# Kernel optimization log

Measured on AMD Instinct MI355X. Metric: run time of the kernel, lower is better.

## Reference

```python
import jax, jax.numpy as jnp
import numpy as np

B, T, HID = 2, 2048, 2048
NH, NKV, D = 16, 4, 128
WIN = 512
ROPE_BASE = 10000.0
SCALE = D ** -0.5
EPS = 1e-12


def setup_inputs() -> dict:
    key = jax.random.key(0)
    ks = jax.random.split(key, 5)
    x = jax.random.normal(ks[0], (B, T, HID), dtype=jnp.float32)
    wq = jax.random.normal(ks[1], (HID, NH * D), dtype=jnp.float32) * 0.02
    wk = jax.random.normal(ks[2], (HID, NKV * D), dtype=jnp.float32) * 0.02
    wv = jax.random.normal(ks[3], (HID, NKV * D), dtype=jnp.float32) * 0.02
    wo = jax.random.normal(ks[4], (NH * D, HID), dtype=jnp.float32) * 0.02
    return {"x": x, "wq": wq, "wk": wk, "wv": wv, "wo": wo}


def _rope_tables(t, offset=0):
    inv_freq = 1.0 / (ROPE_BASE ** (jnp.arange(0, D, 2, dtype=jnp.float32) / D))
    pos = jnp.arange(offset, offset + t, dtype=jnp.float32)
    freqs = pos[:, None] * inv_freq[None, :]              # [t, D/2]
    cos = jnp.concatenate([jnp.cos(freqs), jnp.cos(freqs)], axis=-1)  # [t, D]
    sin = jnp.concatenate([jnp.sin(freqs), jnp.sin(freqs)], axis=-1)
    return cos, sin


def _apply_rope(x, cos, sin):
    # x: [B, H, T, D]; rotate-half formulation
    x1, x2 = jnp.split(x, 2, axis=-1)
    rot = jnp.concatenate([-x2, x1], axis=-1)
    return x * cos[None, None] + rot * sin[None, None]


def _l2norm(x):
    n = jnp.sqrt(jnp.sum(x * x, axis=-1, keepdims=True))
    return x / jnp.maximum(n, EPS)


def _forward(x, wq, wk, wv, wo):
    b, t, _ = x.shape
    q = (x @ wq).reshape(b, t, NH, D).transpose(0, 2, 1, 3)    # [B,H,T,D]
    k = (x @ wk).reshape(b, t, NKV, D).transpose(0, 2, 1, 3)   # [B,Hk,T,D]
    v = (x @ wv).reshape(b, t, NKV, D).transpose(0, 2, 1, 3)
    q = _l2norm(q)
    k = _l2norm(k)
    cos, sin = _rope_tables(t, offset=0)
    q = _apply_rope(q, cos, sin)
    k = _apply_rope(k, cos, sin)
    rep = NH // NKV
    k = jnp.repeat(k, rep, axis=1)                             # GQA repeat_interleave
    v = jnp.repeat(v, rep, axis=1)
    i = jnp.arange(t)
    allowed = (i[None, :] <= i[:, None]) & (i[None, :] > i[:, None] - WIN)  # [T,T]
    logits = jnp.einsum("bhid,bhjd->bhij", q, k) * SCALE
    logits = jnp.where(allowed[None, None], logits, -jnp.inf)
    attn = jax.nn.softmax(logits, axis=-1)
    out = jnp.einsum("bhij,bhjd->bhid", attn, v)
    out = out.transpose(0, 2, 1, 3).reshape(b, t, NH * D)
    return out @ wo


def reference(x, wq, wk, wv, wo):
    return _forward(x, wq, wk, wv, wo)
```

## Files before the change

### kernel.cpp

```cpp
#include <hip/hip_runtime.h>
#include <hip/hip_bf16.h>
#include <cstdint>

#define NHQ 16
#define NKVH 4
#define HDIM 128
#define WINSZ 512
#define TSEQ 2048
#define ATTN_SCALE 0.08838834764831845f

typedef __attribute__((ext_vector_type(8))) short s16x8;
typedef __attribute__((ext_vector_type(4))) float f32x4;

__device__ __forceinline__ void gload16(const void* g, void* lds) {
  __builtin_amdgcn_global_load_lds(
      (const __attribute__((address_space(1))) unsigned int*)g,
      (__attribute__((address_space(3))) unsigned int*)(uintptr_t)lds,
      16, 0, 0);
}

__device__ __forceinline__ f32x4 mfma16(s16x8 a, s16x8 b, f32x4 c) {
  return __builtin_amdgcn_mfma_f32_16x16x32_bf16(a, b, c, 0, 0, 0);
}

#define SBAR() asm volatile("s_barrier" ::: "memory")
#define VMCNT(n) asm volatile("s_waitcnt vmcnt(" #n ")" ::: "memory")

__global__ __launch_bounds__(256) void rope_tables_kernel(float* __restrict__ cosT,
                                                          float* __restrict__ sinT) {
  int idx = blockIdx.x * 256 + threadIdx.x;
  int t = idx >> 6, d2 = idx & 63;
  float inv = powf(10000.0f, -(float)d2 / 64.0f);
  float a = (float)t * inv;
  cosT[idx] = cosf(a);
  sinT[idx] = sinf(a);
}

__global__ __launch_bounds__(256) void cast_kernel(const float* __restrict__ in,
                                                   __bf16* __restrict__ out, int n4) {
  int i = blockIdx.x * 256 + threadIdx.x;
  if (i >= n4) return;
  float4 v = ((const float4*)in)[i];
  union { __bf16 h[4]; uint2 u; } pk;
  pk.h[0] = (__bf16)v.x; pk.h[1] = (__bf16)v.y; pk.h[2] = (__bf16)v.z; pk.h[3] = (__bf16)v.w;
  ((uint2*)out)[i] = pk.u;
}

__global__ __launch_bounds__(256) void transpose_cast(const float* __restrict__ in,
                                                      __bf16* __restrict__ out, int R, int C) {
  __shared__ float tile[32][33];
  int c0 = blockIdx.x * 32, r0 = blockIdx.y * 32;
  int tx = threadIdx.x, ty = threadIdx.y;
#pragma unroll
  for (int i = 0; i < 4; i++)
    tile[ty + i * 8][tx] = in[(size_t)(r0 + ty + i * 8) * C + c0 + tx];
  __syncthreads();
#pragma unroll
  for (int i = 0; i < 4; i++)
    out[(size_t)(c0 + ty + i * 8) * R + r0 + tx] = (__bf16)tile[tx][ty + i * 8];
}

template <int MODE>
__global__ __launch_bounds__(512, 2) void gemm256(const __bf16* __restrict__ A,
                                                  const __bf16* __restrict__ Bt,
                                                  float* __restrict__ Cf,
                                                  __bf16* __restrict__ Qo, __bf16* __restrict__ Ko,
                                                  __bf16* __restrict__ Vo, int M, int N, int K) {
  __shared__ __attribute__((aligned(16))) char Lds[3][2][16384];

  const int tid = threadIdx.x;
  const int w = tid >> 6, lane = tid & 63;
  const int wm = w >> 2, wn = w & 3;

  const int nbx = gridDim.x;
  const int nwg = nbx * gridDim.y;
  const int bid = blockIdx.y * nbx + blockIdx.x;
  const int q8 = nwg >> 3, r8 = nwg & 7;
  const int xcd = bid & 7, idx = bid >> 3;
  const int swz = (xcd < r8 ? xcd * (q8 + 1) : r8 * (q8 + 1) + (xcd - r8) * q8) + idx;
  const int bx = swz % nbx, by = swz / nbx;
  const int m0 = by * 256, n0 = bx * 256;

  const int r_st = tid >> 2;
  const int c_src = (tid & 3) ^ ((tid >> 3) & 3);
  const __bf16* gA = A + (size_t)(m0 + r_st) * K + c_src * 8;
  const __bf16* gB = Bt + (size_t)(n0 + r_st) * K + c_src * 8;
  const size_t hOF = (size_t)128 * K;

  auto stA = [&](int t, int h, int b) {
    gload16(gA + h * hOF + t * 32, Lds[b][0] + h * 8192 + w * 1024);
  };
  auto stB = [&](int t, int h, int b) {
    gload16(gB + h * hOF + t * 32, Lds[b][1] + h * 8192 + w * 1024);
  };

  const int swzr = (((lane >> 4) ^ (((lane & 15) >> 1) & 3)) << 4);
  const int aoff = wm * 8192 + (lane & 15) * 64 + swzr;
  const int boff = (wn >> 1) * 8192 + (wn & 1) * 4096 + (lane & 15) * 64 + swzr;

  f32x4 acc[8][4];
  f32x4 zero = {0.f, 0.f, 0.f, 0.f};
#pragma unroll
  for (int i = 0; i < 8; i++)
#pragma unroll
    for (int j = 0; j < 4; j++) acc[i][j] = zero;

  const int NT = K >> 5;

  stA(0, 0, 0); stA(0, 1, 0); stB(0, 0, 0); stB(0, 1, 0);
  stA(1, 0, 1); stA(1, 1, 1); stB(1, 0, 1);
  VMCNT(3);
  SBAR();

  int cur = 0;
  for (int t = 0; t < NT; ++t) {
    int nb1 = cur + 1; if (nb1 == 3) nb1 = 0;
    int nb2 = nb1 + 1; if (nb2 == 3) nb2 = 0;
    const char* bA = Lds[cur][0];
    const char* bB = Lds[cur][1];

    s16x8 fb[4], fa[4];
#pragma unroll
    for (int nf = 0; nf < 4; nf++) fb[nf] = *(const s16x8*)(bB + boff + nf * 1024);
#pragma unroll
    for (int mf = 0; mf < 4; mf++) fa[mf] = *(const s16x8*)(bA + aoff + mf * 1024);
    if (t + 1 < NT) stB(t + 1, 1, nb1);
    if (t + 2 < NT) stA(t + 2, 0, nb2);
    SBAR();
    __builtin_amdgcn_s_setprio(1);
#pragma unroll
    for (int mf = 0; mf < 4; mf++)
#pragma unroll
      for (int nf = 0; nf < 4; nf++) acc[mf][nf] = mfma16(fa[mf], fb[nf], acc[mf][nf]);
    __builtin_amdgcn_s_setprio(0);
    SBAR();

#pragma unroll
    for (int mf = 0; mf < 4; mf++) fa[mf] = *(const s16x8*)(bA + aoff + 4096 + mf * 1024);
    if (t + 2 < NT) { stA(t + 2, 1, nb2); stB(t + 2, 0, nb2); }
    SBAR();
    __builtin_amdgcn_s_setprio(1);
#pragma unroll
    for (int mf = 0; mf < 4; mf++)
#pragma unroll
      for (int nf = 0; nf < 4; nf++) acc[4 + mf][nf] = mfma16(fa[mf], fb[nf], acc[4 + mf][nf]);
    __builtin_amdgcn_s_setprio(0);

    if (t < NT - 2) {
      VMCNT(3);
      SBAR();
    } else if (t == NT - 2) {
      VMCNT(0);
      SBAR();
    }
    cur = nb1;
  }

#pragma unroll
  for (int mf = 0; mf < 8; mf++)
#pragma unroll
    for (int nf = 0; nf < 4; nf++) {
      int rbase = m0 + wm * 128 + mf * 16 + (lane >> 4) * 4;
      int col = n0 + wn * 64 + nf * 16 + (lane & 15);
#pragma unroll
      for (int r = 0; r < 4; r++) {
        int m = rbase + r;
        float v = acc[mf][nf][r];
        if constexpr (MODE == 0) {
          Cf[(size_t)m * N + col] = v;
        } else {
          int b = m >> 11, t = m & 2047;
          __bf16 bv = (__bf16)v;
          if (col < 2048) {
            Qo[(((size_t)(b * NHQ + (col >> 7))) * TSEQ + t) * HDIM + (col & 127)] = bv;
          } else if (col < 2560) {
            int c2 = col - 2048;
            Ko[(((size_t)(b * NKVH + (c2 >> 7))) * TSEQ + t) * HDIM + (c2 & 127)] = bv;
          } else {
            int c2 = col - 2560;
            Vo[(((size_t)(b * NKVH + (c2 >> 7))) * TSEQ + t) * HDIM + (c2 & 127)] = bv;
          }
        }
      }
    }
}

__global__ __launch_bounds__(256) void normrope(__bf16* __restrict__ Q, __bf16* __restrict__ Kk,
                                                const float* __restrict__ cosT,
                                                const float* __restrict__ sinT) {
  int w = threadIdx.x >> 6, lane = threadIdx.x & 63;
  int row = blockIdx.x / 5;
  int slot = (blockIdx.x % 5) * 4 + w;
  int b = row >> 11, t = row & 2047;
  __bf16* p;
  if (slot < 16)
    p = Q + (((size_t)(b * NHQ + slot)) * TSEQ + t) * HDIM;
  else
    p = Kk + (((size_t)(b * NKVH + (slot - 16))) * TSEQ + t) * HDIM;
  float x1 = (float)p[lane], x2 = (float)p[lane + 64];
  float ss = x1 * x1 + x2 * x2;
#pragma unroll
  for (int off = 32; off; off >>= 1) ss += __shfl_xor(ss, off);
  float inv = 1.0f / fmaxf(sqrtf(ss), 1e-12f);
  x1 *= inv;
  x2 *= inv;
  float c = cosT[t * 64 + lane], s = sinT[t * 64 + lane];
  p[lane] = (__bf16)(x1 * c - x2 * s);
  p[lane + 64] = (__bf16)(x2 * c + x1 * s);
}

__global__ __launch_bounds__(256) void attn_kernel(const __bf16* __restrict__ Qf,
                                                   const __bf16* __restrict__ Kf,
                                                   const __bf16* __restrict__ Vf,
                                                   __bf16* __restrict__ Ab) {
  __shared__ __align__(16) __bf16 Kl[32 * 136];
  __shared__ __align__(16) __bf16 Vt[128 * 40];
  __shared__ __align__(16) __bf16 Pl[4][16 * 40];
  int tid = threadIdx.x, w = tid >> 6, lane = tid & 63;
  int bid = blockIdx.x;
  int qt = bid & 31, h = (bid >> 5) & 15, b = bid >> 9;
  int qs = qt * 64;
  int kvh = h >> 2;
  const __bf16* Qb = Qf + ((size_t)(b * NHQ + h) * TSEQ) * HDIM;
  const __bf16* Kb = Kf + ((size_t)(b * NKVH + kvh) * TSEQ) * HDIM;
  const __bf16* Vb = Vf + ((size_t)(b * NKVH + kvh) * TSEQ) * HDIM;

  s16x8 aq[4];
  int qrow_f = qs + w * 16 + (lane & 15);
#pragma unroll
  for (int kb = 0; kb < 4; kb++)
    aq[kb] = *(const s16x8*)(Qb + (size_t)qrow_f * HDIM + kb * 32 + (lane >> 4) * 8);

  f32x4 acc[8];
  f32x4 zero = {0.f, 0.f, 0.f, 0.f};
#pragma unroll
  for (int db = 0; db < 8; db++) acc[db] = zero;
  float mrow[4], lrow[4];
#pragma unroll
  for (int r = 0; r < 4; r++) { mrow[r] = -1e30f; lrow[r] = 0.f; }

  int lo = qs - (WINSZ - 1);
  if (lo < 0) lo = 0;
  lo &= ~31;

  for (int ks = lo; ks <= qs + 63; ks += 32) {
    __syncthreads();
#pragma unroll
    for (int i = 0; i < 2; i++) {
      int c = tid + 256 * i;
      int j = c >> 4, dk = (c & 15) * 8;
      int4 kv = *(const int4*)(Kb + (size_t)(ks + j) * HDIM + dk);
      *(int4*)&Kl[j * 136 + dk] = kv;
      int jv = c & 31, d0 = (c >> 5) * 8;
      int4 vv = *(const int4*)(Vb + (size_t)(ks + jv) * HDIM + d0);
      const __bf16* pv = (const __bf16*)&vv;
#pragma unroll
      for (int e = 0; e < 8; e++) Vt[(d0 + e) * 40 + jv] = pv[e];
    }
    __syncthreads();

    f32x4 sacc[2];
    sacc[0] = zero; sacc[1] = zero;
#pragma unroll
    for (int jb = 0; jb < 2; jb++)
#pragma unroll
      for (int kb = 0; kb < 4; kb++) {
        s16x8 bk = *(const s16x8*)&Kl[(jb * 16 + (lane & 15)) * 136 + kb * 32 + (lane >> 4) * 8];
        sacc[jb] = mfma16(aq[kb], bk, sacc[jb]);
      }

    int colbase = ks + (lane & 15);
    float p0v[4], p1v[4], scf[4];
#pragma unroll
    for (int r = 0; r < 4; r++) {
      int qrow = qs + w * 16 + (lane >> 4) * 4 + r;
      float s0 = sacc[0][r] * ATTN_SCALE, s1 = sacc[1][r] * ATTN_SCALE;
      int j0 = colbase, j1 = colbase + 16;
      bool a0 = (j0 <= qrow) && (j0 > qrow - WINSZ);
      bool a1 = (j1 <= qrow) && (j1 > qrow - WINSZ);
      float mt = fmaxf(a0 ? s0 : -1e30f, a1 ? s1 : -1e30f);
#pragma unroll
      for (int off = 1; off < 16; off <<= 1) mt = fmaxf(mt, __shfl_xor(mt, off));
      float mn = fmaxf(mrow[r], mt);
      float p0 = a0 ? __expf(s0 - mn) : 0.f;
      float p1 = a1 ? __expf(s1 - mn) : 0.f;
      float sf = __expf(mrow[r] - mn);
      float ts = p0 + p1;
#pragma unroll
      for (int off = 1; off < 16; off <<= 1) ts += __shfl_xor(ts, off);
      lrow[r] = lrow[r] * sf + ts;
      mrow[r] = mn;
      p0v[r] = p0; p1v[r] = p1; scf[r] = sf;
    }

#pragma unroll
    for (int r = 0; r < 4; r++) {
      Pl[w][((lane >> 4) * 4 + r) * 40 + 0 * 16 + (lane & 15)] = (__bf16)p0v[r];
      Pl[w][((lane >> 4) * 4 + r) * 40 + 1 * 16 + (lane & 15)] = (__bf16)p1v[r];
    }
#pragma unroll
    for (int db = 0; db < 8; db++) {
      f32x4 t = acc[db];
#pragma unroll
      for (int r = 0; r < 4; r++) t[r] *= scf[r];
      acc[db] = t;
    }

    s16x8 pa = *(const s16x8*)&Pl[w][(lane & 15) * 40 + (lane >> 4) * 8];
#pragma unroll
    for (int db = 0; db < 8; db++) {
      s16x8 bv = *(const s16x8*)&Vt[(db * 16 + (lane & 15)) * 40 + (lane >> 4) * 8];
      acc[db] = mfma16(pa, bv, acc[db]);
    }
  }

#pragma unroll
  for (int db = 0; db < 8; db++)
#pragma unroll
    for (int r = 0; r < 4; r++) {
      int qrow = qs + w * 16 + (lane >> 4) * 4 + r;
      float v = acc[db][r] / lrow[r];
      Ab[((size_t)(b * TSEQ + qrow)) * 2048 + h * HDIM + db * 16 + (lane & 15)] = (__bf16)v;
    }
}

extern "C" void kernel_launch(void* const* d_in, const int* in_sizes, int n_in,
                              void* d_out, int out_size, void* d_ws, size_t ws_size,
                              hipStream_t stream) {
  const float* x = (const float*)d_in[0];
  const float* wq = (const float*)d_in[1];
  const float* wk = (const float*)d_in[2];
  const float* wv = (const float*)d_in[3];
  const float* wo = (const float*)d_in[4];
  float* out = (float*)d_out;

  char* ws = (char*)d_ws;
  size_t off = 0;
  auto alloc = [&](size_t bytes) -> void* {
    void* p = ws + off;
    off += (bytes + 255) & ~(size_t)255;
    return p;
  };
  __bf16* Xb = (__bf16*)alloc((size_t)4096 * 2048 * 2);
  __bf16* Wqkvt = (__bf16*)alloc((size_t)3072 * 2048 * 2);
  __bf16* Wot = (__bf16*)alloc((size_t)2048 * 2048 * 2);
  __bf16* Q = (__bf16*)alloc((size_t)2 * NHQ * TSEQ * HDIM * 2);
  __bf16* Kb = (__bf16*)alloc((size_t)2 * NKVH * TSEQ * HDIM * 2);
  __bf16* Vb = (__bf16*)alloc((size_t)2 * NKVH * TSEQ * HDIM * 2);
  float* cosT = (float*)alloc((size_t)TSEQ * 64 * 4);
  float* sinT = (float*)alloc((size_t)TSEQ * 64 * 4);
  __bf16* Ab = Xb;

  rope_tables_kernel<<<TSEQ * 64 / 256, 256, 0, stream>>>(cosT, sinT);
  cast_kernel<<<8192, 256, 0, stream>>>(x, Xb, 2097152);
  dim3 tb(32, 8);
  transpose_cast<<<dim3(64, 64), tb, 0, stream>>>(wq, Wqkvt, 2048, 2048);
  transpose_cast<<<dim3(16, 64), tb, 0, stream>>>(wk, Wqkvt + (size_t)2048 * 2048, 2048, 512);
  transpose_cast<<<dim3(16, 64), tb, 0, stream>>>(wv, Wqkvt + (size_t)2560 * 2048, 2048, 512);
  transpose_cast<<<dim3(64, 64), tb, 0, stream>>>(wo, Wot, 2048, 2048);

  gemm256<1><<<dim3(12, 16), 512, 0, stream>>>(Xb, Wqkvt, nullptr, Q, Kb, Vb, 4096, 3072, 2048);
  normrope<<<4096 * 5, 256, 0, stream>>>(Q, Kb, cosT, sinT);
  attn_kernel<<<2 * NHQ * (TSEQ / 64), 256, 0, stream>>>(Q, Kb, Vb, Ab);
  gemm256<0><<<dim3(8, 16), 512, 0, stream>>>(Ab, Wot, out, nullptr, nullptr, nullptr, 4096, 2048,
                                              2048);
}
```

Measured before the change: 240.4 us.

## Deepen GEMM pipeline to four LDS stages and narrow output-projection tiles

The GEMM kernel now uses four LDS buffers with a prefetch distance of three K-steps instead of three buffers and distance two, and waits on vmcnt values derived from the per-step load count. It is also templated on the N-fragment count, so the output projection runs with 256x128 tiles and a 256-workgroup grid in place of 128 workgroups. This targets memory latency and poor CU occupancy on the smaller GEMM. In exchange it uses more LDS per workgroup, which may limit residency of two blocks per CU, and the narrower tiles reuse A less.

```diff
diff --git a/kernel.cpp b/kernel.cpp
--- a/kernel.cpp
+++ b/kernel.cpp
@@ -25,6 +25,15 @@
 
 #define SBAR() asm volatile("s_barrier" ::: "memory")
 #define VMCNT(n) asm volatile("s_waitcnt vmcnt(" #n ")" ::: "memory")
+
+template <int N>
+__device__ __forceinline__ void vmwait() {
+  if constexpr (N == 8) VMCNT(8);
+  else if constexpr (N == 6) VMCNT(6);
+  else if constexpr (N == 4) VMCNT(4);
+  else if constexpr (N == 3) VMCNT(3);
+  else VMCNT(0);
+}
 
 __global__ __launch_bounds__(256) void rope_tables_kernel(float* __restrict__ cosT,
                                                           float* __restrict__ sinT) {
@@ -60,13 +69,16 @@
     out[(size_t)(c0 + ty + i * 8) * R + r0 + tx] = (__bf16)tile[tx][ty + i * 8];
 }
 
-template <int MODE>
+template <int MODE, int NF>
 __global__ __launch_bounds__(512, 2) void gemm256(const __bf16* __restrict__ A,
                                                   const __bf16* __restrict__ Bt,
                                                   float* __restrict__ Cf,
                                                   __bf16* __restrict__ Qo, __bf16* __restrict__ Ko,
                                                   __bf16* __restrict__ Vo, int M, int N, int K) {
-  __shared__ __attribute__((aligned(16))) char Lds[3][2][16384];
+  constexpr int BUNITS = NF / 2;
+  constexpr int LPT = 2 + BUNITS;
+  constexpr int STEADY = 2 * LPT;
+  __shared__ __attribute__((aligned(16))) char Lds[4][(2 + BUNITS) * 8192];
 
   const int tid = threadIdx.x;
   const int w = tid >> 6, lane = tid & 63;
@@ -79,7 +91,7 @@
   const int xcd = bid & 7, idx = bid >> 3;
   const int swz = (xcd < r8 ? xcd * (q8 + 1) : r8 * (q8 + 1) + (xcd - r8) * q8) + idx;
   const int bx = swz % nbx, by = swz / nbx;
-  const int m0 = by * 256, n0 = bx * 256;
+  const int m0 = by * 256, n0 = bx * (NF * 64);
 
   const int r_st = tid >> 2;
   const int c_src = (tid & 3) ^ ((tid >> 3) & 3);
@@ -88,80 +100,88 @@
   const size_t hOF = (size_t)128 * K;
 
   auto stA = [&](int t, int h, int b) {
-    gload16(gA + h * hOF + t * 32, Lds[b][0] + h * 8192 + w * 1024);
+    gload16(gA + h * hOF + t * 32, Lds[b] + h * 8192 + w * 1024);
   };
-  auto stB = [&](int t, int h, int b) {
-    gload16(gB + h * hOF + t * 32, Lds[b][1] + h * 8192 + w * 1024);
+  auto stB = [&](int t, int u, int b) {
+    gload16(gB + u * hOF + t * 32, Lds[b] + 16384 + u * 8192 + w * 1024);
   };
 
   const int swzr = (((lane >> 4) ^ (((lane & 15) >> 1) & 3)) << 4);
   const int aoff = wm * 8192 + (lane & 15) * 64 + swzr;
-  const int boff = (wn >> 1) * 8192 + (wn & 1) * 4096 + (lane & 15) * 64 + swzr;
-
-  f32x4 acc[8][4];
+  const int boff = (NF == 4 ? ((wn >> 1) * 8192 + (wn & 1) * 4096) : wn * 2048) +
+                   (lane & 15) * 64 + swzr;
+
+  f32x4 acc[8][NF];
   f32x4 zero = {0.f, 0.f, 0.f, 0.f};
 #pragma unroll
   for (int i = 0; i < 8; i++)
 #pragma unroll
-    for (int j = 0; j < 4; j++) acc[i][j] = zero;
+    for (int j = 0; j < NF; j++) acc[i][j] = zero;
 
   const int NT = K >> 5;
 
-  stA(0, 0, 0); stA(0, 1, 0); stB(0, 0, 0); stB(0, 1, 0);
-  stA(1, 0, 1); stA(1, 1, 1); stB(1, 0, 1);
-  VMCNT(3);
+#pragma unroll
+  for (int t = 0; t < 3; t++) {
+    stA(t, 0, t); stA(t, 1, t);
+#pragma unroll
+    for (int u = 0; u < BUNITS; u++) stB(t, u, t);
+  }
+  vmwait<STEADY>();
   SBAR();
 
-  int cur = 0;
   for (int t = 0; t < NT; ++t) {
-    int nb1 = cur + 1; if (nb1 == 3) nb1 = 0;
-    int nb2 = nb1 + 1; if (nb2 == 3) nb2 = 0;
-    const char* bA = Lds[cur][0];
-    const char* bB = Lds[cur][1];
-
-    s16x8 fb[4], fa[4];
-#pragma unroll
-    for (int nf = 0; nf < 4; nf++) fb[nf] = *(const s16x8*)(bB + boff + nf * 1024);
+    const int cur = t & 3, nb = (t + 3) & 3;
+    const bool more = (t + 3) < NT;
+    const char* bA = Lds[cur];
+    const char* bB = Lds[cur] + 16384;
+
+    s16x8 fb[NF], fa[4];
+#pragma unroll
+    for (int nf = 0; nf < NF; nf++) fb[nf] = *(const s16x8*)(bB + boff + nf * 1024);
 #pragma unroll
     for (int mf = 0; mf < 4; mf++) fa[mf] = *(const s16x8*)(bA + aoff + mf * 1024);
-    if (t + 1 < NT) stB(t + 1, 1, nb1);
-    if (t + 2 < NT) stA(t + 2, 0, nb2);
+    if (more) { stA(t + 3, 0, nb); stA(t + 3, 1, nb); }
     SBAR();
     __builtin_amdgcn_s_setprio(1);
 #pragma unroll
     for (int mf = 0; mf < 4; mf++)
 #pragma unroll
-      for (int nf = 0; nf < 4; nf++) acc[mf][nf] = mfma16(fa[mf], fb[nf], acc[mf][nf]);
+      for (int nf = 0; nf < NF; nf++) acc[mf][nf] = mfma16(fa[mf], fb[nf], acc[mf][nf]);
     __builtin_amdgcn_s_setprio(0);
     SBAR();
 
 #pragma unroll
     for (int mf = 0; mf < 4; mf++) fa[mf] = *(const s16x8*)(bA + aoff + 4096 + mf * 1024);
-    if (t + 2 < NT) { stA(t + 2, 1, nb2); stB(t + 2, 0, nb2); }
+    if (more) {
+#pragma unroll
+      for (int u = 0; u < BUNITS; u++) stB(t + 3, u, nb);
+    }
     SBAR();
     __builtin_amdgcn_s_setprio(1);
 #pragma unroll
     for (int mf = 0; mf < 4; mf++)
 #pragma unroll
-      for (int nf = 0; nf < 4; nf++) acc[4 + mf][nf] = mfma16(fa[mf], fb[nf], acc[4 + mf][nf]);
+      for (int nf = 0; nf < NF; nf++) acc[4 + mf][nf] = mfma16(fa[mf], fb[nf], acc[4 + mf][nf]);
     __builtin_amdgcn_s_setprio(0);
 
-    if (t < NT - 2) {
-      VMCNT(3);
+    if (t < NT - 3) {
+      vmwait<STEADY>();
+      SBAR();
+    } else if (t == NT - 3) {
+      vmwait<LPT>();
       SBAR();
     } else if (t == NT - 2) {
       VMCNT(0);
       SBAR();
     }
-    cur = nb1;
   }
 
 #pragma unroll
   for (int mf = 0; mf < 8; mf++)
 #pragma unroll
-    for (int nf = 0; nf < 4; nf++) {
+    for (int nf = 0; nf < NF; nf++) {
       int rbase = m0 + wm * 128 + mf * 16 + (lane >> 4) * 4;
-      int col = n0 + wn * 64 + nf * 16 + (lane & 15);
+      int col = n0 + wn * (NF * 16) + nf * 16 + (lane & 15);
 #pragma unroll
       for (int r = 0; r < 4; r++) {
         int m = rbase + r;
@@ -359,9 +379,9 @@
   transpose_cast<<<dim3(16, 64), tb, 0, stream>>>(wv, Wqkvt + (size_t)2560 * 2048, 2048, 512);
   transpose_cast<<<dim3(64, 64), tb, 0, stream>>>(wo, Wot, 2048, 2048);
 
-  gemm256<1><<<dim3(12, 16), 512, 0, stream>>>(Xb, Wqkvt, nullptr, Q, Kb, Vb, 4096, 3072, 2048);
+  gemm256<1, 4><<<dim3(12, 16), 512, 0, stream>>>(Xb, Wqkvt, nullptr, Q, Kb, Vb, 4096, 3072, 2048);
   normrope<<<4096 * 5, 256, 0, stream>>>(Q, Kb, cosT, sinT);
   attn_kernel<<<2 * NHQ * (TSEQ / 64), 256, 0, stream>>>(Q, Kb, Vb, Ab);
-  gemm256<0><<<dim3(8, 16), 512, 0, stream>>>(Ab, Wot, out, nullptr, nullptr, nullptr, 4096, 2048,
-                                              2048);
-}
+  gemm256<0, 2><<<dim3(16, 16), 512, 0, stream>>>(Ab, Wot, out, nullptr, nullptr, nullptr, 4096,
+                                                  2048, 2048);
+}
```

Measured after the change: 222.1 us. 7.6% less time.

## Retile GEMMs to 256x128 with 4-stage LDS pipeline and register double-buffering

Applied to the files above, without the earlier changes.

Replaces the 256x256 three-buffer GEMM with a 256x128 tile that uses a four-deep LDS ring, three-stage-ahead global prefetch, and ping-pong register fragments. This lets LDS reads for the next k-step overlap the current MFMA block. The smaller tile doubles the grid (384 and 256 workgroups) for better CU fill on 256 CUs, at the cost of more global traffic per FLOP and fewer accumulators per wave. Wave layout changes to 4x2 with 64x64 per wave.

```diff
diff --git a/kernel.cpp b/kernel.cpp
--- a/kernel.cpp
+++ b/kernel.cpp
@@ -25,6 +25,7 @@
 
 #define SBAR() asm volatile("s_barrier" ::: "memory")
 #define VMCNT(n) asm volatile("s_waitcnt vmcnt(" #n ")" ::: "memory")
+#define LGKM(n) asm volatile("s_waitcnt lgkmcnt(" #n ")" ::: "memory")
 
 __global__ __launch_bounds__(256) void rope_tables_kernel(float* __restrict__ cosT,
                                                           float* __restrict__ sinT) {
@@ -61,16 +62,16 @@
 }
 
 template <int MODE>
-__global__ __launch_bounds__(512, 2) void gemm256(const __bf16* __restrict__ A,
-                                                  const __bf16* __restrict__ Bt,
-                                                  float* __restrict__ Cf,
-                                                  __bf16* __restrict__ Qo, __bf16* __restrict__ Ko,
-                                                  __bf16* __restrict__ Vo, int M, int N, int K) {
-  __shared__ __attribute__((aligned(16))) char Lds[3][2][16384];
+__global__ __launch_bounds__(512, 2) void gemmP(const __bf16* __restrict__ A,
+                                                const __bf16* __restrict__ Bt,
+                                                float* __restrict__ Cf,
+                                                __bf16* __restrict__ Qo, __bf16* __restrict__ Ko,
+                                                __bf16* __restrict__ Vo, int M, int N, int K) {
+  __shared__ __attribute__((aligned(16))) char Lds[4][24576];
 
   const int tid = threadIdx.x;
   const int w = tid >> 6, lane = tid & 63;
-  const int wm = w >> 2, wn = w & 3;
+  const int wm = w >> 1, wn = w & 1;
 
   const int nbx = gridDim.x;
   const int nwg = nbx * gridDim.y;
@@ -79,88 +80,82 @@
   const int xcd = bid & 7, idx = bid >> 3;
   const int swz = (xcd < r8 ? xcd * (q8 + 1) : r8 * (q8 + 1) + (xcd - r8) * q8) + idx;
   const int bx = swz % nbx, by = swz / nbx;
-  const int m0 = by * 256, n0 = bx * 256;
+  const int m0 = by * 256, n0 = bx * 128;
 
   const int r_st = tid >> 2;
   const int c_src = (tid & 3) ^ ((tid >> 3) & 3);
   const __bf16* gA = A + (size_t)(m0 + r_st) * K + c_src * 8;
   const __bf16* gB = Bt + (size_t)(n0 + r_st) * K + c_src * 8;
-  const size_t hOF = (size_t)128 * K;
-
-  auto stA = [&](int t, int h, int b) {
-    gload16(gA + h * hOF + t * 32, Lds[b][0] + h * 8192 + w * 1024);
+  const size_t uOF = (size_t)128 * K;
+
+  auto stage = [&](int t) {
+    char* b = Lds[t & 3] + w * 1024;
+    gload16(gA + t * 32, b);
+    gload16(gA + uOF + t * 32, b + 8192);
+    gload16(gB + t * 32, b + 16384);
   };
-  auto stB = [&](int t, int h, int b) {
-    gload16(gB + h * hOF + t * 32, Lds[b][1] + h * 8192 + w * 1024);
-  };
 
   const int swzr = (((lane >> 4) ^ (((lane & 15) >> 1) & 3)) << 4);
-  const int aoff = wm * 8192 + (lane & 15) * 64 + swzr;
-  const int boff = (wn >> 1) * 8192 + (wn & 1) * 4096 + (lane & 15) * 64 + swzr;
-
-  f32x4 acc[8][4];
+  const int aoff = (wm >> 1) * 8192 + (wm & 1) * 4096 + (lane & 15) * 64 + swzr;
+  const int boff = 16384 + wn * 4096 + (lane & 15) * 64 + swzr;
+
+  f32x4 acc[4][4];
   f32x4 zero = {0.f, 0.f, 0.f, 0.f};
 #pragma unroll
-  for (int i = 0; i < 8; i++)
+  for (int i = 0; i < 4; i++)
 #pragma unroll
     for (int j = 0; j < 4; j++) acc[i][j] = zero;
 
   const int NT = K >> 5;
 
-  stA(0, 0, 0); stA(0, 1, 0); stB(0, 0, 0); stB(0, 1, 0);
-  stA(1, 0, 1); stA(1, 1, 1); stB(1, 0, 1);
-  VMCNT(3);
+  s16x8 faE[4], fbE[4], faO[4], fbO[4];
+
+  stage(0); stage(1); stage(2);
+  VMCNT(6);
   SBAR();
-
-  int cur = 0;
-  for (int t = 0; t < NT; ++t) {
-    int nb1 = cur + 1; if (nb1 == 3) nb1 = 0;
-    int nb2 = nb1 + 1; if (nb2 == 3) nb2 = 0;
-    const char* bA = Lds[cur][0];
-    const char* bB = Lds[cur][1];
-
-    s16x8 fb[4], fa[4];
-#pragma unroll
-    for (int nf = 0; nf < 4; nf++) fb[nf] = *(const s16x8*)(bB + boff + nf * 1024);
-#pragma unroll
-    for (int mf = 0; mf < 4; mf++) fa[mf] = *(const s16x8*)(bA + aoff + mf * 1024);
-    if (t + 1 < NT) stB(t + 1, 1, nb1);
-    if (t + 2 < NT) stA(t + 2, 0, nb2);
-    SBAR();
-    __builtin_amdgcn_s_setprio(1);
-#pragma unroll
-    for (int mf = 0; mf < 4; mf++)
-#pragma unroll
-      for (int nf = 0; nf < 4; nf++) acc[mf][nf] = mfma16(fa[mf], fb[nf], acc[mf][nf]);
-    __builtin_amdgcn_s_setprio(0);
-    SBAR();
-
-#pragma unroll
-    for (int mf = 0; mf < 4; mf++) fa[mf] = *(const s16x8*)(bA + aoff + 4096 + mf * 1024);
-    if (t + 2 < NT) { stA(t + 2, 1, nb2); stB(t + 2, 0, nb2); }
-    SBAR();
-    __builtin_amdgcn_s_setprio(1);
-#pragma unroll
-    for (int mf = 0; mf < 4; mf++)
-#pragma unroll
-      for (int nf = 0; nf < 4; nf++) acc[4 + mf][nf] = mfma16(fa[mf], fb[nf], acc[4 + mf][nf]);
-    __builtin_amdgcn_s_setprio(0);
-
-    if (t < NT - 2) {
-      VMCNT(3);
-      SBAR();
-    } else if (t == NT - 2) {
-      VMCNT(0);
-      SBAR();
-    }
-    cur = nb1;
+  {
+    const char* bT = Lds[0];
+#pragma unroll
+    for (int i = 0; i < 4; i++) faE[i] = *(const s16x8*)(bT + aoff + i * 1024);
+#pragma unroll
+    for (int i = 0; i < 4; i++) fbE[i] = *(const s16x8*)(bT + boff + i * 1024);
   }
 
-#pragma unroll
-  for (int mf = 0; mf < 8; mf++)
+#define REGION(TT, FAU, FBU, FAR, FBR)                                        \
+  {                                                                           \
+    const int tt = (TT);                                                      \
+    if (tt + 1 < NT) {                                                        \
+      const char* bT = Lds[(tt + 1) & 3];                                     \
+      _Pragma("unroll") for (int i = 0; i < 4; i++)                           \
+          FAR[i] = *(const s16x8*)(bT + aoff + i * 1024);                     \
+      _Pragma("unroll") for (int i = 0; i < 4; i++)                           \
+          FBR[i] = *(const s16x8*)(bT + boff + i * 1024);                     \
+    }                                                                         \
+    if (tt + 3 < NT) stage(tt + 3);                                           \
+    if (tt + 1 < NT) { LGKM(8); } else { LGKM(0); }                           \
+    __builtin_amdgcn_sched_barrier(0);                                        \
+    __builtin_amdgcn_s_setprio(1);                                            \
+    _Pragma("unroll") for (int mf = 0; mf < 4; mf++)                          \
+      _Pragma("unroll") for (int nf = 0; nf < 4; nf++)                        \
+          acc[mf][nf] = mfma16(FAU[mf], FBU[nf], acc[mf][nf]);                \
+    __builtin_amdgcn_s_setprio(0);                                            \
+    if (tt + 2 < NT) {                                                        \
+      if (tt + 3 < NT) { VMCNT(3); } else { VMCNT(0); }                       \
+      SBAR();                                                                 \
+    }                                                                         \
+  }
+
+  for (int t = 0; t < NT; t += 2) {
+    REGION(t, faE, fbE, faO, fbO);
+    REGION(t + 1, faO, fbO, faE, fbE);
+  }
+#undef REGION
+
+#pragma unroll
+  for (int mf = 0; mf < 4; mf++)
 #pragma unroll
     for (int nf = 0; nf < 4; nf++) {
-      int rbase = m0 + wm * 128 + mf * 16 + (lane >> 4) * 4;
+      int rbase = m0 + wm * 64 + mf * 16 + (lane >> 4) * 4;
       int col = n0 + wn * 64 + nf * 16 + (lane & 15);
 #pragma unroll
       for (int r = 0; r < 4; r++) {
@@ -359,9 +354,9 @@
   transpose_cast<<<dim3(16, 64), tb, 0, stream>>>(wv, Wqkvt + (size_t)2560 * 2048, 2048, 512);
   transpose_cast<<<dim3(64, 64), tb, 0, stream>>>(wo, Wot, 2048, 2048);
 
-  gemm256<1><<<dim3(12, 16), 512, 0, stream>>>(Xb, Wqkvt, nullptr, Q, Kb, Vb, 4096, 3072, 2048);
+  gemmP<1><<<dim3(24, 16), 512, 0, stream>>>(Xb, Wqkvt, nullptr, Q, Kb, Vb, 4096, 3072, 2048);
   normrope<<<4096 * 5, 256, 0, stream>>>(Q, Kb, cosT, sinT);
   attn_kernel<<<2 * NHQ * (TSEQ / 64), 256, 0, stream>>>(Q, Kb, Vb, Ab);
-  gemm256<0><<<dim3(8, 16), 512, 0, stream>>>(Ab, Wot, out, nullptr, nullptr, nullptr, 4096, 2048,
-                                              2048);
-}
+  gemmP<0><<<dim3(16, 16), 512, 0, stream>>>(Ab, Wot, out, nullptr, nullptr, nullptr, 4096, 2048,
+                                             2048);
+}
```

Result: faster. 225.3 us (-6.3%).

## Restructure GEMM to K=64 double-buffered tiles with four-phase MFMA schedule

Applied to the files above, without the earlier changes.

Replaces the triple-buffered K=32 GEMM mainloop with a double-buffered K=64 tile (64KB LDS per stage) and a new XOR swizzle. Each iteration is split into four quadrant MFMA phases, with global-to-LDS loads for tile t+2 interleaved between them and explicit lgkmcnt waits plus sched barriers. The aim is to halve the loop-iteration and barrier count per K and to overlap loads better with MFMA. In exchange it uses more LDS per block, which may limit occupancy, and it adds more barriers per iteration.

```diff
diff --git a/kernel.cpp b/kernel.cpp
--- a/kernel.cpp
+++ b/kernel.cpp
@@ -25,6 +25,7 @@
 
 #define SBAR() asm volatile("s_barrier" ::: "memory")
 #define VMCNT(n) asm volatile("s_waitcnt vmcnt(" #n ")" ::: "memory")
+#define LGKM(n) asm volatile("s_waitcnt lgkmcnt(" #n ")" ::: "memory")
 
 __global__ __launch_bounds__(256) void rope_tables_kernel(float* __restrict__ cosT,
                                                           float* __restrict__ sinT) {
@@ -61,12 +62,12 @@
 }
 
 template <int MODE>
-__global__ __launch_bounds__(512, 2) void gemm256(const __bf16* __restrict__ A,
-                                                  const __bf16* __restrict__ Bt,
-                                                  float* __restrict__ Cf,
-                                                  __bf16* __restrict__ Qo, __bf16* __restrict__ Ko,
-                                                  __bf16* __restrict__ Vo, int M, int N, int K) {
-  __shared__ __attribute__((aligned(16))) char Lds[3][2][16384];
+__global__ __launch_bounds__(512, 2) void gemm8(const __bf16* __restrict__ A,
+                                                const __bf16* __restrict__ Bt,
+                                                float* __restrict__ Cf,
+                                                __bf16* __restrict__ Qo, __bf16* __restrict__ Ko,
+                                                __bf16* __restrict__ Vo, int M, int N, int K) {
+  __shared__ __attribute__((aligned(16))) char Lds[2][65536];
 
   const int tid = threadIdx.x;
   const int w = tid >> 6, lane = tid & 63;
@@ -81,22 +82,23 @@
   const int bx = swz % nbx, by = swz / nbx;
   const int m0 = by * 256, n0 = bx * 256;
 
-  const int r_st = tid >> 2;
-  const int c_src = (tid & 3) ^ ((tid >> 3) & 3);
-  const __bf16* gA = A + (size_t)(m0 + r_st) * K + c_src * 8;
-  const __bf16* gB = Bt + (size_t)(n0 + r_st) * K + c_src * 8;
-  const size_t hOF = (size_t)128 * K;
-
-  auto stA = [&](int t, int h, int b) {
-    gload16(gA + h * hOF + t * 32, Lds[b][0] + h * 8192 + w * 1024);
+  const int ru = tid >> 3;
+  const int cs = (tid & 7) ^ (ru & 7);
+  const __bf16* gAs = A + (size_t)(m0 + ru) * K + cs * 8;
+  const __bf16* gBs = Bt + (size_t)(n0 + ru) * K + cs * 8;
+
+  auto stA = [&](int tt, int u) {
+    gload16(gAs + (size_t)(64 * u) * K + tt * 64, Lds[tt & 1] + u * 8192 + w * 1024);
   };
-  auto stB = [&](int t, int h, int b) {
-    gload16(gB + h * hOF + t * 32, Lds[b][1] + h * 8192 + w * 1024);
+  auto stB = [&](int tt, int u) {
+    gload16(gBs + (size_t)(64 * u) * K + tt * 64, Lds[tt & 1] + 32768 + u * 8192 + w * 1024);
   };
 
-  const int swzr = (((lane >> 4) ^ (((lane & 15) >> 1) & 3)) << 4);
-  const int aoff = wm * 8192 + (lane & 15) * 64 + swzr;
-  const int boff = (wn >> 1) * 8192 + (wn & 1) * 4096 + (lane & 15) * 64 + swzr;
+  const int rowb = (lane & 15) * 128;
+  const int cph0 = (((lane >> 4)) ^ (lane & 7)) * 16;
+  const int cph1 = ((4 + (lane >> 4)) ^ (lane & 7)) * 16;
+  const int Abase = wm * 16384;
+  const int Bbase = 32768 + wn * 8192;
 
   f32x4 acc[8][4];
   f32x4 zero = {0.f, 0.f, 0.f, 0.f};
@@ -105,55 +107,106 @@
 #pragma unroll
     for (int j = 0; j < 4; j++) acc[i][j] = zero;
 
-  const int NT = K >> 5;
-
-  stA(0, 0, 0); stA(0, 1, 0); stB(0, 0, 0); stB(0, 1, 0);
-  stA(1, 0, 1); stA(1, 1, 1); stB(1, 0, 1);
-  VMCNT(3);
+  const int NT = K >> 6;
+
+#pragma unroll
+  for (int u = 0; u < 4; u++) stA(0, u);
+#pragma unroll
+  for (int u = 0; u < 4; u++) stB(0, u);
+#pragma unroll
+  for (int u = 0; u < 4; u++) stA(1, u);
+#pragma unroll
+  for (int u = 0; u < 4; u++) stB(1, u);
+  VMCNT(8);
   SBAR();
 
-  int cur = 0;
+  s16x8 fa[4][2], fb[4][2];
+
   for (int t = 0; t < NT; ++t) {
-    int nb1 = cur + 1; if (nb1 == 3) nb1 = 0;
-    int nb2 = nb1 + 1; if (nb2 == 3) nb2 = 0;
-    const char* bA = Lds[cur][0];
-    const char* bB = Lds[cur][1];
-
-    s16x8 fb[4], fa[4];
-#pragma unroll
-    for (int nf = 0; nf < 4; nf++) fb[nf] = *(const s16x8*)(bB + boff + nf * 1024);
-#pragma unroll
-    for (int mf = 0; mf < 4; mf++) fa[mf] = *(const s16x8*)(bA + aoff + mf * 1024);
-    if (t + 1 < NT) stB(t + 1, 1, nb1);
-    if (t + 2 < NT) stA(t + 2, 0, nb2);
-    SBAR();
+    const char* bs = Lds[t & 1];
+    const bool more = (t + 2) < NT;
+
+#pragma unroll
+    for (int mi = 0; mi < 4; mi++) {
+      fa[mi][0] = *(const s16x8*)(bs + Abase + mi * 2048 + rowb + cph0);
+      fa[mi][1] = *(const s16x8*)(bs + Abase + mi * 2048 + rowb + cph1);
+    }
+#pragma unroll
+    for (int ni = 0; ni < 2; ni++) {
+      fb[ni][0] = *(const s16x8*)(bs + Bbase + ni * 2048 + rowb + cph0);
+      fb[ni][1] = *(const s16x8*)(bs + Bbase + ni * 2048 + rowb + cph1);
+    }
+    SBAR();
+    LGKM(0);
+    __builtin_amdgcn_sched_barrier(0);
     __builtin_amdgcn_s_setprio(1);
 #pragma unroll
-    for (int mf = 0; mf < 4; mf++)
-#pragma unroll
-      for (int nf = 0; nf < 4; nf++) acc[mf][nf] = mfma16(fa[mf], fb[nf], acc[mf][nf]);
+    for (int mi = 0; mi < 4; mi++)
+#pragma unroll
+      for (int ni = 0; ni < 2; ni++)
+#pragma unroll
+        for (int kk = 0; kk < 2; kk++)
+          acc[mi][ni] = mfma16(fa[mi][kk], fb[ni][kk], acc[mi][ni]);
     __builtin_amdgcn_s_setprio(0);
     SBAR();
 
 #pragma unroll
-    for (int mf = 0; mf < 4; mf++) fa[mf] = *(const s16x8*)(bA + aoff + 4096 + mf * 1024);
-    if (t + 2 < NT) { stA(t + 2, 1, nb2); stB(t + 2, 0, nb2); }
-    SBAR();
+    for (int ni = 2; ni < 4; ni++) {
+      fb[ni][0] = *(const s16x8*)(bs + Bbase + ni * 2048 + rowb + cph0);
+      fb[ni][1] = *(const s16x8*)(bs + Bbase + ni * 2048 + rowb + cph1);
+    }
+    if (more) { stA(t + 2, 0); stA(t + 2, 2); }
+    SBAR();
+    LGKM(0);
+    __builtin_amdgcn_sched_barrier(0);
     __builtin_amdgcn_s_setprio(1);
 #pragma unroll
-    for (int mf = 0; mf < 4; mf++)
-#pragma unroll
-      for (int nf = 0; nf < 4; nf++) acc[4 + mf][nf] = mfma16(fa[mf], fb[nf], acc[4 + mf][nf]);
+    for (int mi = 0; mi < 4; mi++)
+#pragma unroll
+      for (int ni = 2; ni < 4; ni++)
+#pragma unroll
+        for (int kk = 0; kk < 2; kk++)
+          acc[mi][ni] = mfma16(fa[mi][kk], fb[ni][kk], acc[mi][ni]);
     __builtin_amdgcn_s_setprio(0);
-
-    if (t < NT - 2) {
-      VMCNT(3);
-      SBAR();
-    } else if (t == NT - 2) {
+    SBAR();
+
+#pragma unroll
+    for (int mi = 0; mi < 4; mi++) {
+      fa[mi][0] = *(const s16x8*)(bs + Abase + 8192 + mi * 2048 + rowb + cph0);
+      fa[mi][1] = *(const s16x8*)(bs + Abase + 8192 + mi * 2048 + rowb + cph1);
+    }
+    if (more) { stB(t + 2, 0); stB(t + 2, 1); stB(t + 2, 2); stB(t + 2, 3); }
+    SBAR();
+    LGKM(0);
+    __builtin_amdgcn_sched_barrier(0);
+    __builtin_amdgcn_s_setprio(1);
+#pragma unroll
+    for (int mi = 0; mi < 4; mi++)
+#pragma unroll
+      for (int ni = 0; ni < 2; ni++)
+#pragma unroll
+        for (int kk = 0; kk < 2; kk++)
+          acc[4 + mi][ni] = mfma16(fa[mi][kk], fb[ni][kk], acc[4 + mi][ni]);
+    __builtin_amdgcn_s_setprio(0);
+    SBAR();
+
+    if (more) { stA(t + 2, 1); stA(t + 2, 3); }
+    if (t + 2 < NT) {
+      VMCNT(8);
+    } else if (t + 1 < NT) {
       VMCNT(0);
-      SBAR();
-    }
-    cur = nb1;
+    }
+    SBAR();
+    __builtin_amdgcn_s_setprio(1);
+#pragma unroll
+    for (int mi = 0; mi < 4; mi++)
+#pragma unroll
+      for (int ni = 2; ni < 4; ni++)
+#pragma unroll
+        for (int kk = 0; kk < 2; kk++)
+          acc[4 + mi][ni] = mfma16(fa[mi][kk], fb[ni][kk], acc[4 + mi][ni]);
+    __builtin_amdgcn_s_setprio(0);
+    SBAR();
   }
 
 #pragma unroll
@@ -169,16 +222,16 @@
         if constexpr (MODE == 0) {
           Cf[(size_t)m * N + col] = v;
         } else {
-          int b = m >> 11, t = m & 2047;
+          int b = m >> 11, tq = m & 2047;
           __bf16 bv = (__bf16)v;
           if (col < 2048) {
-            Qo[(((size_t)(b * NHQ + (col >> 7))) * TSEQ + t) * HDIM + (col & 127)] = bv;
+            Qo[(((size_t)(b * NHQ + (col >> 7))) * TSEQ + tq) * HDIM + (col & 127)] = bv;
           } else if (col < 2560) {
             int c2 = col - 2048;
-            Ko[(((size_t)(b * NKVH + (c2 >> 7))) * TSEQ + t) * HDIM + (c2 & 127)] = bv;
+            Ko[(((size_t)(b * NKVH + (c2 >> 7))) * TSEQ + tq) * HDIM + (c2 & 127)] = bv;
           } else {
             int c2 = col - 2560;
-            Vo[(((size_t)(b * NKVH + (c2 >> 7))) * TSEQ + t) * HDIM + (c2 & 127)] = bv;
+            Vo[(((size_t)(b * NKVH + (c2 >> 7))) * TSEQ + tq) * HDIM + (c2 & 127)] = bv;
           }
         }
       }
@@ -359,9 +412,9 @@
   transpose_cast<<<dim3(16, 64), tb, 0, stream>>>(wv, Wqkvt + (size_t)2560 * 2048, 2048, 512);
   transpose_cast<<<dim3(64, 64), tb, 0, stream>>>(wo, Wot, 2048, 2048);
 
-  gemm256<1><<<dim3(12, 16), 512, 0, stream>>>(Xb, Wqkvt, nullptr, Q, Kb, Vb, 4096, 3072, 2048);
+  gemm8<1><<<dim3(12, 16), 512, 0, stream>>>(Xb, Wqkvt, nullptr, Q, Kb, Vb, 4096, 3072, 2048);
   normrope<<<4096 * 5, 256, 0, stream>>>(Q, Kb, cosT, sinT);
   attn_kernel<<<2 * NHQ * (TSEQ / 64), 256, 0, stream>>>(Q, Kb, Vb, Ab);
-  gemm256<0><<<dim3(8, 16), 512, 0, stream>>>(Ab, Wot, out, nullptr, nullptr, nullptr, 4096, 2048,
-                                              2048);
-}
+  gemm8<0><<<dim3(8, 16), 512, 0, stream>>>(Ab, Wot, out, nullptr, nullptr, nullptr, 4096, 2048,
+                                            2048);
+}
```

Result: faster. 233.2 us (-3.0%).
